# Kernel optimization log

Hardware: AMD Instinct MI355X
Metric: run time of the kernel (lower is better)

Reference implementation:

```python
import jax, jax.numpy as jnp
import numpy as np

N, E = 50000, 800000
F_NODE, F_EDGE, H, LAT, MAXN = 128, 16, 128, 64, 200


def setup_inputs() -> dict:
    key = jax.random.key(0)
    ks = jax.random.split(key, 40)
    s = 0.05
    p = {
        'x': jax.random.normal(ks[0], (N, F_NODE), jnp.float32),
        'edge_index': jax.random.randint(ks[1], (2, E), 0, N, jnp.int64),
        'edge_attr': jax.random.normal(ks[2], (E, F_EDGE), jnp.float32),
        'eps': jax.random.normal(ks[3], (1, LAT), jnp.float32),
        'num_nodes': N,
        # GATConv layer 1 (heads=1)
        'W1': jax.random.normal(ks[4], (F_NODE, H), jnp.float32) * s,
        'att_src1': jax.random.normal(ks[5], (H,), jnp.float32) * s,
        'att_dst1': jax.random.normal(ks[6], (H,), jnp.float32) * s,
        'We1': jax.random.normal(ks[7], (F_EDGE, H), jnp.float32) * s,
        'att_e1': jax.random.normal(ks[8], (H,), jnp.float32) * s,
        'b1': jnp.zeros((H,), jnp.float32),
        # GATConv layer 2
        'W2': jax.random.normal(ks[9], (H, H), jnp.float32) * s,
        'att_src2': jax.random.normal(ks[10], (H,), jnp.float32) * s,
        'att_dst2': jax.random.normal(ks[11], (H,), jnp.float32) * s,
        'We2': jax.random.normal(ks[12], (F_EDGE, H), jnp.float32) * s,
        'att_e2': jax.random.normal(ks[13], (H,), jnp.float32) * s,
        'b2': jnp.zeros((H,), jnp.float32),
        # heads
        'mu_W': jax.random.normal(ks[14], (H, LAT), jnp.float32) * s,
        'mu_b': jnp.zeros((LAT,), jnp.float32),
        'lv_W': jax.random.normal(ks[15], (H, LAT), jnp.float32) * s,
        'lv_b': jnp.zeros((LAT,), jnp.float32),
        'dec_W': jax.random.normal(ks[16], (LAT, H), jnp.float32) * s,
        'dec_b': jnp.zeros((H,), jnp.float32),
        'adj_W1': jax.random.normal(ks[17], (H, H), jnp.float32) * s,
        'adj_b1': jnp.zeros((H,), jnp.float32),
        'adj_W2': jax.random.normal(ks[18], (H, MAXN), jnp.float32) * s,
        'adj_b2': jnp.zeros((MAXN,), jnp.float32),
        'nd_W1': jax.random.normal(ks[19], (H, H), jnp.float32) * s,
        'nd_b1': jnp.zeros((H,), jnp.float32),
        'nd_W2': jax.random.normal(ks[20], (H, F_NODE), jnp.float32) * s,
        'nd_b2': jnp.zeros((F_NODE,), jnp.float32),
    }
    return p


def _gat(h, src, dst, ea, W, a_s, a_d, We, a_e, b, n):
    # PyG GATConv, heads=1: linear transform, per-edge attention, segment softmax over dst
    g = h @ W                                     # [n, H]
    alpha = jax.nn.leaky_relu((g @ a_s)[src] + (g @ a_d)[dst] + (ea @ We) @ a_e,
                              negative_slope=0.2)  # [E']
    m = jax.ops.segment_max(alpha, dst, num_segments=n)
    ex = jnp.exp(alpha - m[dst])
    den = jax.ops.segment_sum(ex, dst, num_segments=n)
    w = ex / den[dst]
    return jax.ops.segment_sum(w[:, None] * g[src], dst, num_segments=n) + b


def _forward(x, edge_index, edge_attr, eps, num_nodes,
             W1, att_src1, att_dst1, We1, att_e1, b1,
             W2, att_src2, att_dst2, We2, att_e2, b2,
             mu_W, mu_b, lv_W, lv_b, dec_W, dec_b,
             adj_W1, adj_b1, adj_W2, adj_b2, nd_W1, nd_b1, nd_W2, nd_b2):
    n = x.shape[0]
    src, dst = edge_index[0], edge_index[1]
    # add self loops; self-loop edge_attr = per-node mean of incoming edge_attr (PyG fill_value='mean')
    deg = jax.ops.segment_sum(jnp.ones((src.shape[0],), x.dtype), dst, num_segments=n)
    mean_ea = jax.ops.segment_sum(edge_attr, dst, num_segments=n) / jnp.maximum(deg, 1.0)[:, None]
    loop = jnp.arange(n)
    src_f = jnp.concatenate([src, loop])
    dst_f = jnp.concatenate([dst, loop])
    ea_f = jnp.concatenate([edge_attr, mean_ea])
    h = jax.nn.relu(_gat(x, src_f, dst_f, ea_f, W1, att_src1, att_dst1, We1, att_e1, b1, n))
    h = jax.nn.relu(_gat(h, src_f, dst_f, ea_f, W2, att_src2, att_dst2, We2, att_e2, b2, n))
    hg = h.mean(axis=0, keepdims=True)            # global_mean_pool, single graph -> [1, H]
    mu = hg @ mu_W + mu_b
    logvar = hg @ lv_W + lv_b
    z = mu + eps * jnp.exp(0.5 * logvar)
    hd = jax.nn.relu(z @ dec_W + dec_b)           # [1, H]
    hn = jnp.broadcast_to(hd[:, None, :], (1, num_nodes, hd.shape[-1]))
    adj = jax.nn.relu(hn @ adj_W1 + adj_b1) @ adj_W2 + adj_b2   # [1, n, MAXN]
    adj = adj[:, :, :num_nodes]
    nodes = jax.nn.relu(hn @ nd_W1 + nd_b1) @ nd_W2 + nd_b2     # [1, n, F_NODE]
    return adj, nodes, mu, logvar


def reference(x, edge_index, edge_attr, eps, num_nodes,
              W1, att_src1, att_dst1, We1, att_e1, b1,
              W2, att_src2, att_dst2, We2, att_e2, b2,
              mu_W, mu_b, lv_W, lv_b, dec_W, dec_b,
              adj_W1, adj_b1, adj_W2, adj_b2, nd_W1, nd_b1, nd_W2, nd_b2):
    return _forward(x, edge_index, edge_attr, eps, num_nodes,
                    W1, att_src1, att_dst1, We1, att_e1, b1,
                    W2, att_src2, att_dst2, We2, att_e2, b2,
                    mu_W, mu_b, lv_W, lv_b, dec_W, dec_b,
                    adj_W1, adj_b1, adj_W2, adj_b2, nd_W1, nd_b1, nd_W2, nd_b2)
```

## Files before the change

kernel.cpp:

```cpp
#include <hip/hip_runtime.h>
#include <math.h>

#define NN   50000
#define EE   800000
#define EF   850000
#define HH   128
#define FE   16
#define LATD 64
#define MAXNN 200

#define ADJ_TOT   10000000
#define NODES_TOT 6400000
#define OUT_TOT   16400000
#define MU_OFF    16400000
#define LV_OFF    16400064

#define SCATBLOCKS 3125
#define GEMMBLOCKS 782

typedef __attribute__((ext_vector_type(8))) short bf16x8;
typedef __attribute__((ext_vector_type(4))) float f32x4;
typedef __attribute__((ext_vector_type(2))) float f32x2;

__device__ __forceinline__ unsigned short f2bf(float f){
  unsigned int u = __float_as_uint(f);
  unsigned int r = (u + 0x7FFFu + ((u>>16)&1u)) >> 16;
  return (unsigned short)r;
}
__device__ __forceinline__ float bf2f(unsigned short h){
  return __uint_as_float(((unsigned int)h)<<16);
}
__device__ __forceinline__ float rlanef(float v, int k){
  return __int_as_float(__builtin_amdgcn_readlane(__float_as_int(v), k));
}

__global__ __launch_bounds__(256) void kdegsetup(const int* __restrict__ ei, int* ideg,
                       unsigned short* __restrict__ erank,
                       const float* We1, const float* ae1, const float* We2, const float* ae2,
                       float* wa1, float* wa2,
                       const float* W1, const float* W2,
                       unsigned short* Wp1, unsigned short* Wp2){
  int i = blockIdx.x*256 + threadIdx.x;
  if(i < EE) erank[i] = (unsigned short)atomicAdd(&ideg[ei[EE+i]], 1);
  if(i < FE){
    float s1=0.f, s2=0.f;
    for(int j=0;j<HH;j++){ s1 += We1[i*HH+j]*ae1[j]; s2 += We2[i*HH+j]*ae2[j]; }
    wa1[i]=s1; wa2[i]=s2;
  }
  if(i < HH*HH){
    int n = i >> 7, k = i & 127;
    Wp1[i] = f2bf(W1[k*HH + n]);
    Wp2[i] = f2bf(W2[k*HH + n]);
  }
}

__global__ void kscan1(const int* __restrict__ ideg, int* rowstart, int* blocksum){
  __shared__ int sd[1024];
  int t=threadIdx.x; int i=blockIdx.x*1024+t;
  int v = (i<NN)? (ideg[i]+1) : 0;
  sd[t]=v; __syncthreads();
  for(int off=1; off<1024; off<<=1){
    int x = (t>=off)? sd[t-off] : 0;
    __syncthreads();
    sd[t] += x;
    __syncthreads();
  }
  if(i<NN) rowstart[i] = sd[t]-v;
  if(t==1023) blocksum[blockIdx.x]=sd[1023];
}
__global__ void kscan2(const int* __restrict__ blocksum, int* __restrict__ blockoff, int nb){
  int t = threadIdx.x;
  int v = (t<nb)? blocksum[t] : 0;
  int inc = v;
  #pragma unroll
  for(int off=1; off<64; off<<=1){
    int x = __shfl_up(inc, off);
    if(t>=off) inc += x;
  }
  if(t<=nb) blockoff[t] = inc - v;
}
__global__ void kscan3(int* rowstart, const int* __restrict__ blockoff, int nb){
  int i=blockIdx.x*blockDim.x+threadIdx.x;
  if(i<NN) rowstart[i]+=blockoff[i>>10];
  if(i==0) rowstart[NN]=blockoff[nb];
}

__device__ __forceinline__ void scatter_body(int e,
                         const int* __restrict__ ei, const float* __restrict__ ea,
                         const float* __restrict__ wa1, const float* __restrict__ wa2,
                         const int* __restrict__ rowstart, const unsigned short* __restrict__ erank,
                         uint2* __restrict__ csr){
  if(e>=EE) return;
  int s=ei[e], d=ei[EE+e];
  const float4* ea4 = (const float4*)(ea + (size_t)e*FE);
  float4 v0=ea4[0], v1=ea4[1], v2=ea4[2], v3=ea4[3];
  float va[16]={v0.x,v0.y,v0.z,v0.w, v1.x,v1.y,v1.z,v1.w,
                v2.x,v2.y,v2.z,v2.w, v3.x,v3.y,v3.z,v3.w};
  float d1=0.f,d2=0.f;
  #pragma unroll
  for(int f=0;f<FE;f++){ d1+=va[f]*wa1[f]; d2+=va[f]*wa2[f]; }
  int pos = rowstart[d] + (int)erank[e];
  uint2 en; en.x = (unsigned)s;
  en.y = (unsigned)f2bf(d1) | ((unsigned)f2bf(d2)<<16);
  csr[pos] = en;
}

__device__ __forceinline__ void gemm_body(int bid, int tid, const void* __restrict__ hin, int h_is_fp32,
    const unsigned short* __restrict__ Wp,
    const float* __restrict__ atts, const float* __restrict__ attd,
    unsigned char* __restrict__ A8, float* __restrict__ asrc, float* __restrict__ adst){
  int lane = tid & 63;
  int wid  = tid >> 6;
  int l = lane & 15, q = lane >> 4;
  int r0 = bid*64 + wid*16;
  if(r0 >= NN) return;
  const unsigned short* hb = (const unsigned short*)hin;
  const float*          hf = (const float*)hin;
  int row = r0 + l;

  f32x4 acc[8];
  #pragma unroll
  for(int t=0;t<8;t++) acc[t]=(f32x4){0.f,0.f,0.f,0.f};

  #pragma unroll
  for(int kb=0;kb<4;kb++){
    bf16x8 a;
    if(h_is_fp32){
      const float* p = hf + (size_t)row*HH + kb*32 + q*8;
      float4 u0 = *(const float4*)(p);
      float4 u1 = *(const float4*)(p+4);
      a[0]=(short)f2bf(u0.x); a[1]=(short)f2bf(u0.y); a[2]=(short)f2bf(u0.z); a[3]=(short)f2bf(u0.w);
      a[4]=(short)f2bf(u1.x); a[5]=(short)f2bf(u1.y); a[6]=(short)f2bf(u1.z); a[7]=(short)f2bf(u1.w);
    } else {
      a = *(const bf16x8*)(hb + (size_t)row*HH + kb*32 + q*8);
    }
    #pragma unroll
    for(int t=0;t<8;t++){
      bf16x8 b = *(const bf16x8*)(Wp + (size_t)(t*16+l)*HH + kb*32 + q*8);
      acc[t] = __builtin_amdgcn_mfma_f32_16x16x32_bf16(a, b, acc[t], 0,0,0);
    }
  }

  float av[8], dv[8];
  #pragma unroll
  for(int t=0;t<8;t++){ av[t]=atts[t*16+l]; dv[t]=attd[t*16+l]; }
  #pragma unroll
  for(int reg=0;reg<4;reg++){
    float ps=0.f, pd=0.f;
    #pragma unroll
    for(int t=0;t<8;t++){ ps+=acc[t][reg]*av[t]; pd+=acc[t][reg]*dv[t]; }
    #pragma unroll
    for(int m=8;m>=1;m>>=1){ ps+=__shfl_xor(ps,m,16); pd+=__shfl_xor(pd,m,16); }
    if(l==0){ int R=r0+q*4+reg; asrc[R]=ps; adst[R]=pd; }
  }
  #pragma unroll
  for(int t=0;t<8;t++)
    #pragma unroll
    for(int reg=0;reg<4;reg++){
      int pk = __builtin_amdgcn_cvt_pk_fp8_f32(acc[t][reg], 0.f, 0, false);
      A8[(size_t)(r0+q*4+reg)*HH + t*16 + l] = (unsigned char)(pk & 0xFF);
    }
}

__global__ __launch_bounds__(256) void kgemm3(const void* __restrict__ hin, int h_is_fp32,
    const unsigned short* __restrict__ Wp,
    const float* __restrict__ atts, const float* __restrict__ attd,
    unsigned char* __restrict__ A8, float* __restrict__ asrc, float* __restrict__ adst){
  gemm_body(blockIdx.x, threadIdx.x, hin, h_is_fp32, Wp, atts, attd, A8, asrc, adst);
}

__global__ __launch_bounds__(256) void kscatgemm(
    const int* __restrict__ ei, const float* __restrict__ ea,
    const float* __restrict__ wa1, const float* __restrict__ wa2,
    const int* __restrict__ rowstart, const unsigned short* __restrict__ erank,
    uint2* __restrict__ csr,
    const void* __restrict__ hin, int h_is_fp32,
    const unsigned short* __restrict__ Wp,
    const float* __restrict__ atts, const float* __restrict__ attd,
    unsigned char* __restrict__ A8, float* __restrict__ asrc, float* __restrict__ adst){
  if(blockIdx.x < SCATBLOCKS){
    scatter_body(blockIdx.x*256 + threadIdx.x, ei, ea, wa1, wa2, rowstart, erank, csr);
  } else {
    gemm_body(blockIdx.x - SCATBLOCKS, threadIdx.x, hin, h_is_fp32, Wp, atts, attd, A8, asrc, adst);
  }
}

__global__ __launch_bounds__(256) void kgat(const unsigned char* __restrict__ A8,
    const float* __restrict__ asrc, const float* __restrict__ adst,
    const int* __restrict__ rowstart, const uint2* __restrict__ csr,
    int etsel, const float* __restrict__ bias,
    float* __restrict__ alphabuf, int* __restrict__ srcbuf,
    unsigned short* __restrict__ Bout){
  int lane = threadIdx.x & 63;
  int wid  = threadIdx.x >> 6;
  int i = blockIdx.x*4 + wid;
  if(i >= NN) return;
  int base = rowstart[i];
  int len  = rowstart[i+1]-base;
  float adi = adst[i];
  float a0=0.f, a1=0.f;

  if(__builtin_expect(len <= 64, 1)){
    int s = i; float et = 0.f;
    if(lane < len-1){
      uint2 en = csr[base+lane];
      s = (int)en.x;
      et = etsel ? bf2f((unsigned short)(en.y>>16)) : bf2f((unsigned short)(en.y & 0xFFFFu));
    }
    float ets = (lane < len-1) ? et : 0.f;
    #pragma unroll
    for(int mk=32;mk>=1;mk>>=1) ets += __shfl_xor(ets,mk);
    if(lane == len-1) et = ets / fmaxf((float)(len-1), 1.f);
    float a = -1e30f;
    if(lane < len){
      a = asrc[s] + adi + et;
      a = fmaxf(a, 0.2f*a);
    }
    float m = a;
    #pragma unroll
    for(int mk=32;mk>=1;mk>>=1) m = fmaxf(m, __shfl_xor(m,mk));
    float ex = (lane<len) ? __expf(a-m) : 0.f;
    float sm = ex;
    #pragma unroll
    for(int mk=32;mk>=1;mk>>=1) sm += __shfl_xor(sm,mk);
    ex *= __builtin_amdgcn_rcpf(sm);

    #pragma unroll 4
    for(int k=0;k<len;k++){
      int   sk = __builtin_amdgcn_readlane(s, k);
      float wk = rlanef(ex, k);
      unsigned u = *(const unsigned short*)(A8 + (size_t)sk*HH + lane*2);
      f32x2 v = __builtin_amdgcn_cvt_pk_f32_fp8((int)u, false);
      a0 += wk*v[0]; a1 += wk*v[1];
    }
  } else {
    int deg = len-1;
    float lm = -1e30f, ets = 0.f;
    for(int k=lane;k<deg;k+=64){
      uint2 en = csr[base+k];
      int sr = (int)en.x;
      float et = etsel ? bf2f((unsigned short)(en.y>>16)) : bf2f((unsigned short)(en.y & 0xFFFFu));
      ets += et;
      float a = asrc[sr] + adi + et;
      a = fmaxf(a, 0.2f*a);
      alphabuf[base+k]=a; srcbuf[base+k]=sr;
      lm = fmaxf(lm,a);
    }
    #pragma unroll
    for(int mk=32;mk>=1;mk>>=1){
      ets += __shfl_xor(ets,mk);
      lm   = fmaxf(lm, __shfl_xor(lm,mk));
    }
    float aself = asrc[i] + adi + ets/(float)deg;
    aself = fmaxf(aself, 0.2f*aself);
    lm = fmaxf(lm, aself);
    float ls=0.f;
    for(int k=lane;k<len;k+=64){
      float a = (k<deg)? alphabuf[base+k] : aself;
      float e_ = __expf(a-lm);
      alphabuf[base+k]=e_;
      ls += e_;
    }
    #pragma unroll
    for(int mk=32;mk>=1;mk>>=1) ls += __shfl_xor(ls,mk);
    float inv = 1.f/ls;
    for(int k0=0;k0<len;k0+=64){
      int kk = k0+lane;
      int sv = 0; float ev = 0.f;
      if(kk<len){
        sv = (kk<deg)? srcbuf[base+kk] : i;
        ev = alphabuf[base+kk]*inv;
      }
      int nmax = len-k0; if(nmax>64) nmax=64;
      #pragma unroll 4
      for(int j=0;j<nmax;j++){
        int   sk = __builtin_amdgcn_readlane(sv, j);
        float wk = rlanef(ev, j);
        unsigned u = *(const unsigned short*)(A8 + (size_t)sk*HH + lane*2);
        f32x2 v = __builtin_amdgcn_cvt_pk_f32_fp8((int)u, false);
        a0 += wk*v[0]; a1 += wk*v[1];
      }
    }
  }

  float2 bv = *(const float2*)(bias + lane*2);
  float o0 = fmaxf(a0 + bv.x, 0.f);
  float o1 = fmaxf(a1 + bv.y, 0.f);
  unsigned pk = (unsigned)f2bf(o0) | ((unsigned)f2bf(o1)<<16);
  *(unsigned*)(Bout + (size_t)i*HH + lane*2) = pk;
}

__global__ __launch_bounds__(256) void khg(const unsigned short* __restrict__ B, float* hgsum){
  int f = threadIdx.x & 127;
  int half = threadIdx.x >> 7;
  float s=0.f;
  for(int i = blockIdx.x*2+half; i < NN; i += gridDim.x*2)
    s += bf2f(B[(size_t)i*HH + f]);
  __shared__ float sd[256];
  sd[threadIdx.x]=s; __syncthreads();
  if(half==0) atomicAdd(&hgsum[f], sd[threadIdx.x]+sd[threadIdx.x+128]);
}

__global__ __launch_bounds__(256) void kdec(const float* __restrict__ hgsum, const float* __restrict__ eps,
   const float* muW,const float* mub,const float* lvW,const float* lvb,
   const float* decW,const float* decb,
   const float* aW1,const float* ab1,const float* aW2,const float* ab2,
   const float* nW1,const float* nb1,const float* nW2,const float* nb2,
   float* out, float* rowadj, float* rownodes){
  __shared__ float hg[HH], z[LATD], hd[HH], t1[HH], t2[HH];
  int t=threadIdx.x;
  if(t<HH) hg[t]=hgsum[t]*(1.0f/NN);
  __syncthreads();
  if(t<LATD){
    float mu=mub[t], lv=lvb[t];
    #pragma unroll 8
    for(int k=0;k<HH;k++){ mu += hg[k]*muW[k*LATD+t]; lv += hg[k]*lvW[k*LATD+t]; }
    out[MU_OFF+t]=mu; out[LV_OFF+t]=lv;
    z[t]=mu + eps[t]*expf(0.5f*lv);
  }
  __syncthreads();
  if(t<HH){
    float a=decb[t];
    #pragma unroll 8
    for(int k=0;k<LATD;k++) a += z[k]*decW[k*HH+t];
    hd[t]=fmaxf(a,0.f);
  }
  __syncthreads();
  if(t<HH){
    float a=ab1[t];
    #pragma unroll 8
    for(int k=0;k<HH;k++) a += hd[k]*aW1[k*HH+t];
    t1[t]=fmaxf(a,0.f);
  } else {
    int j=t-HH;
    float a=nb1[j];
    #pragma unroll 8
    for(int k=0;k<HH;k++) a += hd[k]*nW1[k*HH+j];
    t2[j]=fmaxf(a,0.f);
  }
  __syncthreads();
  for(int j=t;j<MAXNN;j+=256){
    float a=ab2[j];
    #pragma unroll 8
    for(int k=0;k<HH;k++) a += t1[k]*aW2[k*MAXNN+j];
    rowadj[j]=a;
  }
  if(t<HH){
    float a=nb2[t];
    #pragma unroll 8
    for(int k=0;k<HH;k++) a += t2[k]*nW2[k*HH+t];
    rownodes[t]=a;
  }
}

__global__ __launch_bounds__(256) void kbcast(const float* __restrict__ rowadj,
                                              const float* __restrict__ rownodes,
                                              float* __restrict__ out){
  __shared__ float row[MAXNN+HH];
  int t=threadIdx.x;
  if(t<MAXNN) row[t]=rowadj[t];
  if(t<HH) row[MAXNN+t]=rownodes[t];
  __syncthreads();
  int stride=gridDim.x*blockDim.x;
  const int tot4 = OUT_TOT/4;
  for(int q=blockIdx.x*blockDim.x+t; q<tot4; q+=stride){
    int idx = q*4;
    float4 vv;
    if(idx<ADJ_TOT){
      int j = idx % MAXNN;
      vv = *(const float4*)&row[j];
    } else {
      int j = (idx-ADJ_TOT) & (HH-1);
      vv = *(const float4*)&row[MAXNN+j];
    }
    *(float4*)&out[idx] = vv;
  }
}

extern "C" void kernel_launch(void* const* d_in, const int* in_sizes, int n_in,
                              void* d_out, int out_size, void* d_ws, size_t ws_size,
                              hipStream_t stream){
  const float* x   = (const float*)d_in[0];
  const int*   ei  = (const int*)d_in[1];
  const float* ea  = (const float*)d_in[2];
  const float* eps = (const float*)d_in[3];
  const float* W1  =(const float*)d_in[5];
  const float* as1 =(const float*)d_in[6];
  const float* ad1 =(const float*)d_in[7];
  const float* We1 =(const float*)d_in[8];
  const float* ae1 =(const float*)d_in[9];
  const float* b1  =(const float*)d_in[10];
  const float* W2  =(const float*)d_in[11];
  const float* as2 =(const float*)d_in[12];
  const float* ad2 =(const float*)d_in[13];
  const float* We2 =(const float*)d_in[14];
  const float* ae2 =(const float*)d_in[15];
  const float* b2  =(const float*)d_in[16];
  const float* muW =(const float*)d_in[17];
  const float* mub =(const float*)d_in[18];
  const float* lvW =(const float*)d_in[19];
  const float* lvb =(const float*)d_in[20];
  const float* decW=(const float*)d_in[21];
  const float* decb=(const float*)d_in[22];
  const float* aW1 =(const float*)d_in[23];
  const float* ab1 =(const float*)d_in[24];
  const float* aW2 =(const float*)d_in[25];
  const float* ab2 =(const float*)d_in[26];
  const float* nW1 =(const float*)d_in[27];
  const float* nb1 =(const float*)d_in[28];
  const float* nW2 =(const float*)d_in[29];
  const float* nb2 =(const float*)d_in[30];
  float* out=(float*)d_out;

  char* w=(char*)d_ws;
  unsigned char*  A8  = (unsigned char*)w;  w += (size_t)NN*HH;
  unsigned short* Bbf = (unsigned short*)w; w += (size_t)NN*HH*2;
  unsigned short* Wp1 = (unsigned short*)w; w += (size_t)HH*HH*2;
  unsigned short* Wp2 = (unsigned short*)w; w += (size_t)HH*HH*2;
  uint2*  csr      = (uint2*)w;  w += (size_t)EF*8;
  float*  alphabuf = (float*)w;  w += (size_t)EF*4;
  int*    srcbuf   = (int*)w;    w += (size_t)EF*4;
  unsigned short* erank = (unsigned short*)w; w += (size_t)EE*2;
  int*    rowstart = (int*)w;    w += (size_t)(NN+1)*4;
  int*    ideg     = (int*)w;    w += (size_t)NN*4;
  float*  hgsum    = (float*)w;  w += 128*4;
  float*  asrc     = (float*)w;  w += (size_t)NN*4;
  float*  adst     = (float*)w;  w += (size_t)NN*4;
  float*  wa1      = (float*)w;  w += 16*4;
  float*  wa2      = (float*)w;  w += 16*4;
  float*  rowadj   = (float*)w;  w += 256*4;
  float*  rownodes = (float*)w;  w += 128*4;
  int*    blocksum = (int*)w;    w += 64*4;
  int*    blockoff = (int*)w;    w += 64*4;

  int nb = (NN+1023)/1024;
  int gatblocks  = (NN+3)/4;

  hipMemsetAsync(ideg, 0, (size_t)(NN+128)*4, stream);
  hipLaunchKernelGGL(kdegsetup, dim3((EE+255)/256), dim3(256), 0, stream,
                     ei, ideg, erank, We1, ae1, We2, ae2, wa1, wa2, W1, W2, Wp1, Wp2);
  hipLaunchKernelGGL(kscan1, dim3(nb), dim3(1024), 0, stream, ideg, rowstart, blocksum);
  hipLaunchKernelGGL(kscan2, dim3(1), dim3(64), 0, stream, blocksum, blockoff, nb);
  hipLaunchKernelGGL(kscan3, dim3((NN+255)/256), dim3(256), 0, stream, rowstart, blockoff, nb);
  hipLaunchKernelGGL(kscatgemm, dim3(SCATBLOCKS+GEMMBLOCKS), dim3(256), 0, stream,
                     ei, ea, wa1, wa2, rowstart, erank, csr,
                     (const void*)x, 1, Wp1, as1, ad1, A8, asrc, adst);
  hipLaunchKernelGGL(kgat,  dim3(gatblocks), dim3(256), 0, stream,
                     A8, asrc, adst, rowstart, csr, 0, b1, alphabuf, srcbuf, Bbf);
  hipLaunchKernelGGL(kgemm3, dim3(GEMMBLOCKS), dim3(256), 0, stream,
                     (const void*)Bbf, 0, Wp2, as2, ad2, A8, asrc, adst);
  hipLaunchKernelGGL(kgat,  dim3(gatblocks), dim3(256), 0, stream,
                     A8, asrc, adst, rowstart, csr, 1, b2, alphabuf, srcbuf, Bbf);
  hipLaunchKernelGGL(khg,   dim3(512), dim3(256), 0, stream, Bbf, hgsum);
  hipLaunchKernelGGL(kdec,  dim3(1), dim3(256), 0, stream, hgsum, eps,
                     muW,mub,lvW,lvb,decW,decb,aW1,ab1,aW2,ab2,nW1,nb1,nW2,nb2,
                     out, rowadj, rownodes);
  hipLaunchKernelGGL(kbcast, dim3(2048), dim3(256), 0, stream, rowadj, rownodes, out);
}
```

Before: 465.5 us.

## Split wavefront into four 16-lane groups gathering 8 fp8 features each in GAT aggregation

The GAT aggregation kernel now assigns each wavefront quarter (16 lanes) to a different neighbor, so every lane loads 8 fp8 features with a single 8-byte load instead of 2 bytes per lane per neighbor. Neighbor indices and weights are broadcast with shuffles, six neighbors' loads are batched ahead of the math, and the four partial sums are combined by cross-lane xor reductions before one 16-byte bf16 store. This aims to cut the number of serialized gather iterations and memory instructions per node, at the cost of more registers and extra shuffle work.

```diff
diff --git a/kernel.cpp b/kernel.cpp
--- a/kernel.cpp
+++ b/kernel.cpp
@@ -29,9 +29,6 @@
 }
 __device__ __forceinline__ float bf2f(unsigned short h){
   return __uint_as_float(((unsigned int)h)<<16);
-}
-__device__ __forceinline__ float rlanef(float v, int k){
-  return __int_as_float(__builtin_amdgcn_readlane(__float_as_int(v), k));
 }
 
 __global__ __launch_bounds__(256) void kdegsetup(const int* __restrict__ ei, int* ideg,
@@ -198,7 +195,11 @@
   int base = rowstart[i];
   int len  = rowstart[i+1]-base;
   float adi = adst[i];
-  float a0=0.f, a1=0.f;
+  int lq = lane & 15;
+  int qq = lane >> 4;
+  float av[8];
+  #pragma unroll
+  for(int j=0;j<8;j++) av[j]=0.f;
 
   if(__builtin_expect(len <= 64, 1)){
     int s = i; float et = 0.f;
@@ -225,13 +226,31 @@
     for(int mk=32;mk>=1;mk>>=1) sm += __shfl_xor(sm,mk);
     ex *= __builtin_amdgcn_rcpf(sm);
 
-    #pragma unroll 4
-    for(int k=0;k<len;k++){
-      int   sk = __builtin_amdgcn_readlane(s, k);
-      float wk = rlanef(ex, k);
-      unsigned u = *(const unsigned short*)(A8 + (size_t)sk*HH + lane*2);
-      f32x2 v = __builtin_amdgcn_cvt_pk_f32_fp8((int)u, false);
-      a0 += wk*v[0]; a1 += wk*v[1];
+    int P4 = (len+3)>>2;
+    for(int t0=0; t0<P4; t0+=6){
+      int skv[6]; float w[6];
+      #pragma unroll
+      for(int j=0;j<6;j++){
+        if(t0+j < P4){
+          int idx = 4*(t0+j) + qq;
+          skv[j] = __shfl(s, idx);
+          w[j]   = __shfl(ex, idx);
+        } else { skv[j] = i; w[j] = 0.f; }
+      }
+      unsigned ux[6], uy[6];
+      #pragma unroll
+      for(int j=0;j<6;j++){
+        uint2 u = *(const uint2*)(A8 + (size_t)skv[j]*HH + lq*8);
+        ux[j]=u.x; uy[j]=u.y;
+      }
+      #pragma unroll
+      for(int j=0;j<6;j++){
+        f32x2 v;
+        v=__builtin_amdgcn_cvt_pk_f32_fp8((int)ux[j],false); av[0]+=w[j]*v[0]; av[1]+=w[j]*v[1];
+        v=__builtin_amdgcn_cvt_pk_f32_fp8((int)ux[j],true ); av[2]+=w[j]*v[0]; av[3]+=w[j]*v[1];
+        v=__builtin_amdgcn_cvt_pk_f32_fp8((int)uy[j],false); av[4]+=w[j]*v[0]; av[5]+=w[j]*v[1];
+        v=__builtin_amdgcn_cvt_pk_f32_fp8((int)uy[j],true ); av[6]+=w[j]*v[0]; av[7]+=w[j]*v[1];
+      }
     }
   } else {
     int deg = len-1;
@@ -264,30 +283,42 @@
     #pragma unroll
     for(int mk=32;mk>=1;mk>>=1) ls += __shfl_xor(ls,mk);
     float inv = 1.f/ls;
-    for(int k0=0;k0<len;k0+=64){
-      int kk = k0+lane;
-      int sv = 0; float ev = 0.f;
-      if(kk<len){
-        sv = (kk<deg)? srcbuf[base+kk] : i;
-        ev = alphabuf[base+kk]*inv;
+    int P4 = (len+3)>>2;
+    for(int t=0;t<P4;t++){
+      int k = 4*t + qq;
+      int sk = i; float wk = 0.f;
+      if(k<len){
+        sk = (k<deg)? srcbuf[base+k] : i;
+        wk = alphabuf[base+k]*inv;
       }
-      int nmax = len-k0; if(nmax>64) nmax=64;
-      #pragma unroll 4
-      for(int j=0;j<nmax;j++){
-        int   sk = __builtin_amdgcn_readlane(sv, j);
-        float wk = rlanef(ev, j);
-        unsigned u = *(const unsigned short*)(A8 + (size_t)sk*HH + lane*2);
-        f32x2 v = __builtin_amdgcn_cvt_pk_f32_fp8((int)u, false);
-        a0 += wk*v[0]; a1 += wk*v[1];
-      }
-    }
-  }
-
-  float2 bv = *(const float2*)(bias + lane*2);
-  float o0 = fmaxf(a0 + bv.x, 0.f);
-  float o1 = fmaxf(a1 + bv.y, 0.f);
-  unsigned pk = (unsigned)f2bf(o0) | ((unsigned)f2bf(o1)<<16);
-  *(unsigned*)(Bout + (size_t)i*HH + lane*2) = pk;
+      uint2 u = *(const uint2*)(A8 + (size_t)sk*HH + lq*8);
+      f32x2 v;
+      v=__builtin_amdgcn_cvt_pk_f32_fp8((int)u.x,false); av[0]+=wk*v[0]; av[1]+=wk*v[1];
+      v=__builtin_amdgcn_cvt_pk_f32_fp8((int)u.x,true ); av[2]+=wk*v[0]; av[3]+=wk*v[1];
+      v=__builtin_amdgcn_cvt_pk_f32_fp8((int)u.y,false); av[4]+=wk*v[0]; av[5]+=wk*v[1];
+      v=__builtin_amdgcn_cvt_pk_f32_fp8((int)u.y,true ); av[6]+=wk*v[0]; av[7]+=wk*v[1];
+    }
+  }
+
+  #pragma unroll
+  for(int j=0;j<8;j++){
+    av[j] += __shfl_xor(av[j],16);
+    av[j] += __shfl_xor(av[j],32);
+  }
+  if(qq==0){
+    const float4* bp = (const float4*)(bias + lq*8);
+    float4 b0=bp[0], b1=bp[1];
+    float o0=fmaxf(av[0]+b0.x,0.f), o1=fmaxf(av[1]+b0.y,0.f);
+    float o2=fmaxf(av[2]+b0.z,0.f), o3=fmaxf(av[3]+b0.w,0.f);
+    float o4=fmaxf(av[4]+b1.x,0.f), o5=fmaxf(av[5]+b1.y,0.f);
+    float o6=fmaxf(av[6]+b1.z,0.f), o7=fmaxf(av[7]+b1.w,0.f);
+    uint4 ov;
+    ov.x=(unsigned)f2bf(o0)|((unsigned)f2bf(o1)<<16);
+    ov.y=(unsigned)f2bf(o2)|((unsigned)f2bf(o3)<<16);
+    ov.z=(unsigned)f2bf(o4)|((unsigned)f2bf(o5)<<16);
+    ov.w=(unsigned)f2bf(o6)|((unsigned)f2bf(o7)<<16);
+    *(uint4*)(Bout + (size_t)i*HH + lq*8) = ov;
+  }
 }
 
 __global__ __launch_bounds__(256) void khg(const unsigned short* __restrict__ B, float* hgsum){
```

Result: faster. 411.1 us (-11.7%).
